# Performance work log

Hardware: AMD Instinct MI355X
Metric: run time of the kernel (lower is better)

The kernel has to match this reference:

```python
import jax, jax.numpy as jnp
import numpy as np

N = 50000      # nodes
E = 800000     # edges
D = 128        # input_dim
H = 128        # hidden_dim
C = 10         # num_classes
G = 1024       # graphs in batch
EPS = 1e-5     # BatchNorm eps


def setup_inputs() -> dict:
    key = jax.random.key(0)
    ks = jax.random.split(key, 16)
    p = lambda k, shape: (jax.random.normal(k, shape, dtype=jnp.float32) * 0.05)
    inp = {
        "x": jax.random.normal(ks[0], (N, D), dtype=jnp.float32),
        "edge_index": jax.random.randint(ks[1], (2, E), 0, N, dtype=jnp.int64),
        "batch": jnp.sort(jax.random.randint(ks[2], (N,), 0, G, dtype=jnp.int64)),
        # GraphConv l: out = x @ w_root + segment_sum(x[src])[dst] @ w_rel + b (PyG GraphConv, aggr='add')
        "w_root1": p(ks[3], (D, H)), "w_rel1": p(ks[4], (D, H)), "b1": p(ks[5], (H,)),
        "w_root2": p(ks[6], (H, H)), "w_rel2": p(ks[7], (H, H)), "b2": p(ks[8], (H,)),
        "w_root3": p(ks[9], (H, H)), "w_rel3": p(ks[10], (H, H)), "b3": p(ks[11], (H,)),
        "g1": jnp.ones((H,), jnp.float32), "be1": jnp.zeros((H,), jnp.float32),
        "g2": jnp.ones((H,), jnp.float32), "be2": jnp.zeros((H,), jnp.float32),
        "g3": jnp.ones((H,), jnp.float32), "be3": jnp.zeros((H,), jnp.float32),
        "w_cls": p(ks[12], (H, C)), "b_cls": p(ks[13], (C,)),
    }
    return inp


def _graph_conv(x, src, dst, w_root, w_rel, b):
    # PyG GraphConv: lin_root(x) + lin_rel(sum_{j in N(i)} x_j) + bias
    agg = jax.ops.segment_sum(x[src], dst, num_segments=N)
    return x @ w_root + agg @ w_rel + b


def _batch_norm(x, gamma, beta):
    mean = jnp.mean(x, axis=0)
    var = jnp.var(x, axis=0)
    return (x - mean) * jax.lax.rsqrt(var + EPS) * gamma + beta


def reference(x, edge_index, batch,
              w_root1, w_rel1, b1, w_root2, w_rel2, b2, w_root3, w_rel3, b3,
              g1, be1, g2, be2, g3, be3, w_cls, b_cls):
    src, dst = edge_index[0], edge_index[1]
    h = jax.nn.relu(_batch_norm(_graph_conv(x, src, dst, w_root1, w_rel1, b1), g1, be1))
    h = jax.nn.relu(_batch_norm(_graph_conv(h, src, dst, w_root2, w_rel2, b2), g2, be2))
    h = _batch_norm(_graph_conv(h, src, dst, w_root3, w_rel3, b3), g3, be3)
    # global_mean_pool over graph ids
    sums = jax.ops.segment_sum(h, batch, num_segments=G)
    counts = jax.ops.segment_sum(jnp.ones((N,), h.dtype), batch, num_segments=G)
    pooled = sums / jnp.maximum(counts, 1.0)[:, None]
    # dropout is identity in eval mode
    return pooled @ w_cls + b_cls
```

## Files before the change

### kernel.cpp

```cpp
#include <hip/hip_runtime.h>


constexpr int   NN   = 50000;
constexpr int   NE   = 800000;
constexpr int   DH   = 128;
constexpr int   NC   = 10;
constexpr int   NG   = 1024;
constexpr float EPSV = 1e-5f;
constexpr int   NB   = (NN + 255) / 256;
constexpr int   NBUK = (NN + 255) / 256;
constexpr int   BCAP = 5120;
constexpr int   EPB  = 8192;
constexpr int   CSB  = (NE + EPB - 1) / EPB;
constexpr int   NSLOT= 32;

typedef __attribute__((ext_vector_type(8))) short bf16x8;
typedef __attribute__((ext_vector_type(4))) float f32x4;

__device__ __forceinline__ float bflo(unsigned u) { return __uint_as_float(u << 16); }
__device__ __forceinline__ float bfhi(unsigned u) { return __uint_as_float(u & 0xffff0000u); }
__device__ __forceinline__ unsigned short f2bf(float f) {
    unsigned u = __float_as_uint(f);
    return (unsigned short)((u + 0x7fffu + ((u >> 16) & 1u)) >> 16);
}
__device__ __forceinline__ unsigned pk2(float a, float b) {
    return (unsigned)f2bf(a) | ((unsigned)f2bf(b) << 16);
}

__global__ __launch_bounds__(256) void coarse_scatter_kernel(
    const int* __restrict__ src, const int* __restrict__ dst,
    int* __restrict__ bukCnt, int2* __restrict__ pairs)
{
    __shared__ int cnt[NBUK], base[NBUK], cur[NBUK];
    const int tid = threadIdx.x;
    const int e0 = blockIdx.x * EPB;
    const int n  = min(EPB, NE - e0);

    for (int b = tid; b < NBUK; b += 256) cnt[b] = 0;
    __syncthreads();
    for (int i = tid; i < n; i += 256)
        atomicAdd(&cnt[dst[e0 + i] >> 8], 1);
    __syncthreads();
    for (int b = tid; b < NBUK; b += 256) {
        base[b] = (cnt[b] > 0) ? atomicAdd(&bukCnt[b], cnt[b]) : 0;
        cur[b] = 0;
    }
    __syncthreads();
    for (int i = tid; i < n; i += 256) {
        int d = dst[e0 + i], s = src[e0 + i];
        int b = d >> 8;
        int r = atomicAdd(&cur[b], 1);
        int p = base[b] + r;
        if (p >= BCAP) p = BCAP - 1;
        pairs[(size_t)b * BCAP + p] = make_int2(s, d);
    }
}

__global__ __launch_bounds__(256) void deg_from_pairs_kernel(
    const int2* __restrict__ pairs, const int* __restrict__ bukCnt,
    int* __restrict__ deg)
{
    __shared__ int cnt[256];
    const int b = blockIdx.x;
    const int tid = threadIdx.x;
    cnt[tid] = 0;
    __syncthreads();
    const int n = min(bukCnt[b], BCAP);
    const int2* p = pairs + (size_t)b * BCAP;
    for (int i = tid; i < n; i += 256)
        atomicAdd(&cnt[p[i].y & 255], 1);
    __syncthreads();
    int node = b * 256 + tid;
    if (node < NN) deg[node] = cnt[tid];
}

__global__ __launch_bounds__(256) void fine_scatter_kernel(
    const int2* __restrict__ pairs, const int* __restrict__ bukCnt,
    int* __restrict__ cursor, int* __restrict__ csr_src)
{
    const int b = blockIdx.x;
    const int tid = threadIdx.x;
    const int n = min(bukCnt[b], BCAP);
    const int2* p = pairs + (size_t)b * BCAP;
    for (int i = tid; i < n; i += 256) {
        int2 e = p[i];
        int pos = atomicAdd(&cursor[e.y], 1);
        csr_src[pos] = e.x;
    }
}

__global__ __launch_bounds__(256) void psum_kernel(
    const int* __restrict__ deg, int* __restrict__ bsum)
{
    int t = threadIdx.x;
    int i = blockIdx.x * 256 + t;
    int d = (i < NN) ? deg[i] : 0;
#pragma unroll
    for (int off = 32; off > 0; off >>= 1) d += __shfl_down(d, off, 64);
    __shared__ int w4[4];
    if ((t & 63) == 0) w4[t >> 6] = d;
    __syncthreads();
    if (t == 0) bsum[blockIdx.x] = w4[0] + w4[1] + w4[2] + w4[3];
}

__global__ __launch_bounds__(256) void scan_bsums_kernel(
    const int* __restrict__ bsum, int* __restrict__ bbase)
{
    __shared__ int tmp[256];
    int t = threadIdx.x;
    int v = (t < NB) ? bsum[t] : 0;
    tmp[t] = v;
    __syncthreads();
    for (int off = 1; off < 256; off <<= 1) {
        int u = (t >= off) ? tmp[t - off] : 0;
        __syncthreads();
        tmp[t] += u;
        __syncthreads();
    }
    if (t < NB) bbase[t] = tmp[t] - v;
}

__global__ __launch_bounds__(256) void offsets_kernel(
    const int* __restrict__ deg, const int* __restrict__ bbase,
    int* __restrict__ offsets, int* __restrict__ cursor)
{
    __shared__ int tmp[256];
    int t = threadIdx.x;
    int i = blockIdx.x * 256 + t;
    int d = (i < NN) ? deg[i] : 0;
    tmp[t] = d;
    __syncthreads();
    for (int off = 1; off < 256; off <<= 1) {
        int u = (t >= off) ? tmp[t - off] : 0;
        __syncthreads();
        tmp[t] += u;
        __syncthreads();
    }
    int incl = tmp[t];
    int base = bbase[blockIdx.x];
    if (i < NN) {
        int o = base + incl - d;
        offsets[i] = o;
        cursor[i]  = o;
        if (i == NN - 1) offsets[NN] = base + incl;
    }
}

__global__ __launch_bounds__(256) void convert_x_kernel(
    const float* __restrict__ x, unsigned short* __restrict__ xb)
{
    int i = blockIdx.x * 256 + threadIdx.x;
    if (i >= NN * DH / 8) return;
    const float4* p = reinterpret_cast<const float4*>(x + (size_t)i * 8);
    float4 v0 = p[0], v1 = p[1];
    uint4 o;
    o.x = pk2(v0.x, v0.y); o.y = pk2(v0.z, v0.w);
    o.z = pk2(v1.x, v1.y); o.w = pk2(v1.z, v1.w);
    *reinterpret_cast<uint4*>(xb + (size_t)i * 8) = o;
}

__global__ __launch_bounds__(256) void transpose_w_kernel(
    const float* __restrict__ w0, const float* __restrict__ w1,
    const float* __restrict__ w2, const float* __restrict__ w3,
    const float* __restrict__ w4, const float* __restrict__ w5,
    unsigned short* __restrict__ t0, unsigned short* __restrict__ t1,
    unsigned short* __restrict__ t2, unsigned short* __restrict__ t3,
    unsigned short* __restrict__ t4, unsigned short* __restrict__ t5)
{
    const float* srcs[6] = {w0, w1, w2, w3, w4, w5};
    unsigned short* dsts[6] = {t0, t1, t2, t3, t4, t5};
    int m = blockIdx.x >> 4;
    int sub = blockIdx.x & 15;
    const float* s = srcs[m];
    unsigned short* d = dsts[m];
    for (int it = 0; it < 4; ++it) {
        int i = sub * 1024 + it * 256 + threadIdx.x;
        int c = i & 127, k = i >> 7;
        d[c * 128 + k] = f2bf(s[k * 128 + c]);
    }
}

template <bool TRANSFORM>
__global__ __launch_bounds__(256) void aggregate_kernel(
    const unsigned short* __restrict__ xb, const int* __restrict__ offsets,
    const int* __restrict__ csr_src, const float* __restrict__ sc,
    const float* __restrict__ sh, unsigned short* __restrict__ aggb)
{
    int tid = blockIdx.x * 256 + threadIdx.x;
    int node = tid >> 4;
    if (node >= NN) return;
    int c8 = (tid & 15) * 8;

    float scv[8], shv[8];
    if (TRANSFORM) {
        float4 a = *reinterpret_cast<const float4*>(sc + c8);
        float4 b = *reinterpret_cast<const float4*>(sc + c8 + 4);
        scv[0]=a.x; scv[1]=a.y; scv[2]=a.z; scv[3]=a.w;
        scv[4]=b.x; scv[5]=b.y; scv[6]=b.z; scv[7]=b.w;
        float4 c = *reinterpret_cast<const float4*>(sh + c8);
        float4 d = *reinterpret_cast<const float4*>(sh + c8 + 4);
        shv[0]=c.x; shv[1]=c.y; shv[2]=c.z; shv[3]=c.w;
        shv[4]=d.x; shv[5]=d.y; shv[6]=d.z; shv[7]=d.w;
    }

    float acc[8] = {0.f,0.f,0.f,0.f,0.f,0.f,0.f,0.f};
    auto addv = [&](uint4 v) {
        float f[8] = {bflo(v.x), bfhi(v.x), bflo(v.y), bfhi(v.y),
                      bflo(v.z), bfhi(v.z), bflo(v.w), bfhi(v.w)};
#pragma unroll
        for (int j = 0; j < 8; ++j) {
            float t = TRANSFORM ? fmaxf(fmaf(f[j], scv[j], shv[j]), 0.f) : f[j];
            acc[j] += t;
        }
    };

    int beg = offsets[node], end = offsets[node + 1];
    int e = beg;
    for (; e + 3 < end; e += 4) {
        int s0 = csr_src[e],     s1 = csr_src[e + 1];
        int s2 = csr_src[e + 2], s3 = csr_src[e + 3];
        uint4 v0 = *reinterpret_cast<const uint4*>(xb + (size_t)s0 * DH + c8);
        uint4 v1 = *reinterpret_cast<const uint4*>(xb + (size_t)s1 * DH + c8);
        uint4 v2 = *reinterpret_cast<const uint4*>(xb + (size_t)s2 * DH + c8);
        uint4 v3 = *reinterpret_cast<const uint4*>(xb + (size_t)s3 * DH + c8);
        addv(v0); addv(v1); addv(v2); addv(v3);
    }
    for (; e < end; ++e)
        addv(*reinterpret_cast<const uint4*>(xb + (size_t)csr_src[e] * DH + c8));

    uint4 o;
    o.x = pk2(acc[0], acc[1]); o.y = pk2(acc[2], acc[3]);
    o.z = pk2(acc[4], acc[5]); o.w = pk2(acc[6], acc[7]);
    *reinterpret_cast<uint4*>(aggb + (size_t)node * DH + c8) = o;
}

template <bool TRANSFORM>
__global__ __launch_bounds__(256, 4) void gemm_mfma_kernel(
    const unsigned short* __restrict__ Xb, const unsigned short* __restrict__ Ab,
    const unsigned short* __restrict__ Wrt, const unsigned short* __restrict__ Wlt,
    const float* __restrict__ bias, const float* __restrict__ scIn,
    const float* __restrict__ shIn, unsigned short* __restrict__ OUTb,
    float* __restrict__ stats)
{
    __shared__ unsigned short sW[128][136];
    __shared__ float sScale[DH], sShift[DH];

    const int tid  = threadIdx.x;
    const int lane = tid & 63;
    const int wave = tid >> 6;
    const int row0 = blockIdx.x * 64;
    const int wrow = wave * 16;
    const int l15  = lane & 15;
    const int lk   = (lane >> 4) * 8;

    if (TRANSFORM && tid < DH) {
        sScale[tid] = scIn[tid];
        sShift[tid] = shIn[tid];
    }
#pragma unroll
    for (int i = 0; i < 8; ++i) {
        int f = i * 256 + tid;
        int c = f >> 4;
        int ks = (f & 15) * 8;
        *reinterpret_cast<uint4*>(&sW[c][ks]) =
            *reinterpret_cast<const uint4*>(Wrt + c * 128 + ks);
    }

    f32x4 acc[8];
#pragma unroll
    for (int nt = 0; nt < 8; ++nt) acc[nt] = (f32x4){0.f, 0.f, 0.f, 0.f};

    const int arow = row0 + wrow + l15;
    const bool valid = arow < NN;
    const unsigned short* xptr = Xb + (size_t)arow * DH + lk;
    const unsigned short* aptr = Ab + (size_t)arow * DH + lk;

    uint4 pre[4];
#pragma unroll
    for (int t = 0; t < 4; ++t)
        pre[t] = valid ? *reinterpret_cast<const uint4*>(xptr + t * 32)
                       : make_uint4(0u, 0u, 0u, 0u);

    __syncthreads();

#pragma unroll
    for (int t = 0; t < 4; ++t) {
        uint4 v = pre[t];
        if (TRANSFORM) {
            int cb = t * 32 + lk;
            float f[8] = {bflo(v.x), bfhi(v.x), bflo(v.y), bfhi(v.y),
                          bflo(v.z), bfhi(v.z), bflo(v.w), bfhi(v.w)};
#pragma unroll
            for (int j = 0; j < 8; ++j)
                f[j] = fmaxf(fmaf(f[j], sScale[cb + j], sShift[cb + j]), 0.f);
            v.x = pk2(f[0], f[1]); v.y = pk2(f[2], f[3]);
            v.z = pk2(f[4], f[5]); v.w = pk2(f[6], f[7]);
        }
        bf16x8 a = *reinterpret_cast<bf16x8*>(&v);
        const int kb = t * 32;
#pragma unroll
        for (int nt = 0; nt < 8; ++nt) {
            bf16x8 b = *reinterpret_cast<const bf16x8*>(&sW[nt * 16 + l15][kb + lk]);
            acc[nt] = __builtin_amdgcn_mfma_f32_16x16x32_bf16(a, b, acc[nt], 0, 0, 0);
        }
    }

#pragma unroll
    for (int t = 0; t < 4; ++t)
        pre[t] = valid ? *reinterpret_cast<const uint4*>(aptr + t * 32)
                       : make_uint4(0u, 0u, 0u, 0u);

    __syncthreads();
#pragma unroll
    for (int i = 0; i < 8; ++i) {
        int f = i * 256 + tid;
        int c = f >> 4;
        int ks = (f & 15) * 8;
        *reinterpret_cast<uint4*>(&sW[c][ks]) =
            *reinterpret_cast<const uint4*>(Wlt + c * 128 + ks);
    }
    __syncthreads();

#pragma unroll
    for (int t = 0; t < 4; ++t) {
        uint4 v = pre[t];
        bf16x8 a = *reinterpret_cast<bf16x8*>(&v);
        const int kb = t * 32;
#pragma unroll
        for (int nt = 0; nt < 8; ++nt) {
            bf16x8 b = *reinterpret_cast<const bf16x8*>(&sW[nt * 16 + l15][kb + lk]);
            acc[nt] = __builtin_amdgcn_mfma_f32_16x16x32_bf16(a, b, acc[nt], 0, 0, 0);
        }
    }

    float s_[8] = {0,0,0,0,0,0,0,0}, q_[8] = {0,0,0,0,0,0,0,0};
#pragma unroll
    for (int nt = 0; nt < 8; ++nt) {
        float bvn = bias[nt * 16 + l15];
#pragma unroll
        for (int r = 0; r < 4; ++r) {
            int orow = row0 + wrow + ((lane >> 4) << 2) + r;
            float o = acc[nt][r] + bvn;
            if (orow < NN) {
                OUTb[(size_t)orow * DH + nt * 16 + l15] = f2bf(o);
                s_[nt] += o;
                q_[nt] += o * o;
            }
        }
    }
#pragma unroll
    for (int nt = 0; nt < 8; ++nt) {
        s_[nt] += __shfl_xor(s_[nt], 16, 64);
        s_[nt] += __shfl_xor(s_[nt], 32, 64);
        q_[nt] += __shfl_xor(q_[nt], 16, 64);
        q_[nt] += __shfl_xor(q_[nt], 32, 64);
    }
    __syncthreads();
    float* ldsS = reinterpret_cast<float*>(&sW[0][0]);
    float* ldsQ = ldsS + 512;
    if (lane < 16) {
#pragma unroll
        for (int nt = 0; nt < 8; ++nt) {
            ldsS[wave * DH + nt * 16 + l15] = s_[nt];
            ldsQ[wave * DH + nt * 16 + l15] = q_[nt];
        }
    }
    __syncthreads();
    if (tid < DH) {
        float s = ldsS[tid] + ldsS[DH + tid] + ldsS[2 * DH + tid] + ldsS[3 * DH + tid];
        float q = ldsQ[tid] + ldsQ[DH + tid] + ldsQ[2 * DH + tid] + ldsQ[3 * DH + tid];
        float* slot = stats + (size_t)(blockIdx.x & (NSLOT - 1)) * 256;
        atomicAdd(&slot[tid], s);
        atomicAdd(&slot[128 + tid], q);
    }
}

__global__ __launch_bounds__(128) void finalize_kernel(
    const float* __restrict__ stats, const float* __restrict__ gamma,
    const float* __restrict__ beta, float* __restrict__ sc,
    float* __restrict__ sh)
{
    int j = threadIdx.x;
    float s = 0.f, q = 0.f;
#pragma unroll 8
    for (int sl = 0; sl < NSLOT; ++sl) {
        s += stats[sl * 256 + j];
        q += stats[sl * 256 + 128 + j];
    }
    float mean = s * (1.f / NN);
    float var  = q * (1.f / NN) - mean * mean;
    float sf = rsqrtf(var + EPSV) * gamma[j];
    sc[j] = sf;
    sh[j] = beta[j] - mean * sf;
}

__global__ __launch_bounds__(256) void ghist_kernel(
    const int* __restrict__ batch, int* __restrict__ gdeg)
{
    int n = blockIdx.x * 256 + threadIdx.x;
    if (n < NN) atomicAdd(&gdeg[batch[n]], 1);
}

__global__ __launch_bounds__(1024) void gscan_kernel(
    const int* __restrict__ gdeg, int* __restrict__ goff)
{
    __shared__ int part[1024];
    int t = threadIdx.x;
    part[t] = gdeg[t];
    __syncthreads();
    for (int off = 1; off < 1024; off <<= 1) {
        int v = (t >= off) ? part[t - off] : 0;
        __syncthreads();
        part[t] += v;
        __syncthreads();
    }
    goff[t + 1] = part[t];
    if (t == 0) goff[0] = 0;
}

__global__ __launch_bounds__(128) void pool_classify_kernel(
    const unsigned short* __restrict__ Hb, const int* __restrict__ goff,
    const float* __restrict__ sc, const float* __restrict__ sh,
    const float* __restrict__ wcls, const float* __restrict__ bcls,
    float* __restrict__ out)
{
    __shared__ float pl[DH];
    int g = blockIdx.x;
    int j = threadIdx.x;
    int beg = goff[g], end = goff[g + 1];
    float s = 0.f;
    for (int n = beg; n < end; ++n)
        s += bflo((unsigned)Hb[(size_t)n * DH + j]);
    float cnt = (float)(end - beg);
    pl[j] = (s * sc[j] + cnt * sh[j]) / fmaxf(cnt, 1.f);
    __syncthreads();
    if (j < NC) {
        float v = bcls[j];
#pragma unroll 16
        for (int k = 0; k < DH; ++k) v += pl[k] * wcls[k * NC + j];
        out[(size_t)g * NC + j] = v;
    }
}

extern "C" void kernel_launch(void* const* d_in, const int* in_sizes, int n_in,
                              void* d_out, int out_size, void* d_ws, size_t ws_size,
                              hipStream_t stream)
{
    const float* x    = (const float*)d_in[0];
    const int*   ei   = (const int*)d_in[1];
    const int*   batch= (const int*)d_in[2];
    const float* wr1  = (const float*)d_in[3];
    const float* wl1  = (const float*)d_in[4];
    const float* b1   = (const float*)d_in[5];
    const float* wr2  = (const float*)d_in[6];
    const float* wl2  = (const float*)d_in[7];
    const float* b2   = (const float*)d_in[8];
    const float* wr3  = (const float*)d_in[9];
    const float* wl3  = (const float*)d_in[10];
    const float* b3   = (const float*)d_in[11];
    const float* g1   = (const float*)d_in[12];
    const float* be1  = (const float*)d_in[13];
    const float* g2   = (const float*)d_in[14];
    const float* be2  = (const float*)d_in[15];
    const float* g3   = (const float*)d_in[16];
    const float* be3  = (const float*)d_in[17];
    const float* wcls = (const float*)d_in[18];
    const float* bcls = (const float*)d_in[19];
    float* out = (float*)d_out;

    const int* srcp = ei;
    const int* dstp = ei + NE;

    char* ws = (char*)d_ws;
    const size_t featB16 = (size_t)NN * DH * sizeof(unsigned short);
    size_t off = 0;
    auto alloc = [&](size_t bytes) {
        void* p = ws + off;
        off += (bytes + 255) & ~(size_t)255;
        return p;
    };
    unsigned short* xb    = (unsigned short*)alloc(featB16);
    unsigned short* aggb  = (unsigned short*)alloc(featB16);
    unsigned short* hAb   = (unsigned short*)alloc(featB16);
    unsigned short* hBb   = (unsigned short*)alloc(featB16);
    unsigned short* wrt1  = (unsigned short*)alloc(DH * DH * 2);
    unsigned short* wlt1  = (unsigned short*)alloc(DH * DH * 2);
    unsigned short* wrt2  = (unsigned short*)alloc(DH * DH * 2);
    unsigned short* wlt2  = (unsigned short*)alloc(DH * DH * 2);
    unsigned short* wrt3  = (unsigned short*)alloc(DH * DH * 2);
    unsigned short* wlt3  = (unsigned short*)alloc(DH * DH * 2);
    float* statsAll = (float*)alloc(3 * NSLOT * 256 * sizeof(float));
    float* stats1 = statsAll;
    float* stats2 = statsAll + NSLOT * 256;
    float* stats3 = statsAll + 2 * NSLOT * 256;
    int*   deg     = (int*)alloc(NN * sizeof(int));
    int*   offsets = (int*)alloc((NN + 1) * sizeof(int));
    int*   cursor  = (int*)alloc(NN * sizeof(int));
    int*   csr_src = (int*)alloc(NE * sizeof(int));
    int2*  pairs   = (int2*)alloc((size_t)NBUK * BCAP * sizeof(int2));
    int*   bukCnt  = (int*)alloc(NBUK * sizeof(int));
    int*   gdeg    = (int*)alloc(NG * sizeof(int));
    int*   goff    = (int*)alloc((NG + 1) * sizeof(int));
    int*   bsum    = (int*)alloc(NB * sizeof(int));
    int*   bbase   = (int*)alloc(NB * sizeof(int));
    float* sc1 = (float*)alloc(DH * 4); float* sh1 = (float*)alloc(DH * 4);
    float* sc2 = (float*)alloc(DH * 4); float* sh2 = (float*)alloc(DH * 4);
    float* sc3 = (float*)alloc(DH * 4); float* sh3 = (float*)alloc(DH * 4);

    const int nodeBlocks = (NN + 255) / 256;
    const int aggBlocks  = (NN * 16 + 255) / 256;
    const int gemmBlocks = (NN + 63) / 64;
    const int cvtBlocks  = (NN * DH / 8 + 255) / 256;

    hipMemsetAsync(statsAll, 0, 3 * NSLOT * 256 * sizeof(float), stream);

    hipMemsetAsync(bukCnt, 0, NBUK * sizeof(int), stream);
    coarse_scatter_kernel<<<CSB, 256, 0, stream>>>(srcp, dstp, bukCnt, pairs);
    deg_from_pairs_kernel<<<NBUK, 256, 0, stream>>>(pairs, bukCnt, deg);
    psum_kernel<<<NB, 256, 0, stream>>>(deg, bsum);
    scan_bsums_kernel<<<1, 256, 0, stream>>>(bsum, bbase);
    offsets_kernel<<<NB, 256, 0, stream>>>(deg, bbase, offsets, cursor);
    fine_scatter_kernel<<<NBUK, 256, 0, stream>>>(pairs, bukCnt, cursor, csr_src);

    hipMemsetAsync(gdeg, 0, NG * sizeof(int), stream);
    ghist_kernel<<<nodeBlocks, 256, 0, stream>>>(batch, gdeg);
    gscan_kernel<<<1, 1024, 0, stream>>>(gdeg, goff);

    convert_x_kernel<<<cvtBlocks, 256, 0, stream>>>(x, xb);
    transpose_w_kernel<<<96, 256, 0, stream>>>(wr1, wl1, wr2, wl2, wr3, wl3,
                                               wrt1, wlt1, wrt2, wlt2, wrt3, wlt3);

    aggregate_kernel<false><<<aggBlocks, 256, 0, stream>>>(xb, offsets, csr_src, nullptr, nullptr, aggb);
    gemm_mfma_kernel<false><<<gemmBlocks, 256, 0, stream>>>(xb, aggb, wrt1, wlt1, b1, nullptr, nullptr, hAb, stats1);
    finalize_kernel<<<1, 128, 0, stream>>>(stats1, g1, be1, sc1, sh1);

    aggregate_kernel<true><<<aggBlocks, 256, 0, stream>>>(hAb, offsets, csr_src, sc1, sh1, aggb);
    gemm_mfma_kernel<true><<<gemmBlocks, 256, 0, stream>>>(hAb, aggb, wrt2, wlt2, b2, sc1, sh1, hBb, stats2);
    finalize_kernel<<<1, 128, 0, stream>>>(stats2, g2, be2, sc2, sh2);

    aggregate_kernel<true><<<aggBlocks, 256, 0, stream>>>(hBb, offsets, csr_src, sc2, sh2, aggb);
    gemm_mfma_kernel<true><<<gemmBlocks, 256, 0, stream>>>(hBb, aggb, wrt3, wlt3, b3, sc2, sh2, hAb, stats3);
    finalize_kernel<<<1, 128, 0, stream>>>(stats3, g3, be3, sc3, sh3);

    pool_classify_kernel<<<NG, 128, 0, stream>>>(hAb, goff, sc3, sh3, wcls, bcls, out);
}
```

Baseline: 259.9 us.

## Slice aggregation by feature quarters and compute graph offsets by binary search

The aggregate kernel now gives each block 64 nodes and one 32-column quarter of the features, with 4 threads per node instead of 16 threads covering all 128 columns. This narrows each gather row to 64 bytes and should improve cache locality per slice, at the cost of reading the CSR indices four times. Graph offsets are now found by a binary search over the sorted batch array, which replaces the histogram, memset and scan kernels with a single small launch. That search depends on batch being sorted, as the reference input is.

```diff
diff --git a/kernel.cpp b/kernel.cpp
--- a/kernel.cpp
+++ b/kernel.cpp
@@ -146,6 +146,19 @@
     }
 }
 
+__global__ __launch_bounds__(256) void goff_kernel(
+    const int* __restrict__ batch, int* __restrict__ goff)
+{
+    int g = blockIdx.x * 256 + threadIdx.x;
+    if (g > NG) return;
+    int lo = 0, hi = NN;
+    while (lo < hi) {
+        int mid = (lo + hi) >> 1;
+        if (batch[mid] < g) lo = mid + 1; else hi = mid;
+    }
+    goff[g] = lo;
+}
+
 __global__ __launch_bounds__(256) void convert_x_kernel(
     const float* __restrict__ x, unsigned short* __restrict__ xb)
 {
@@ -186,10 +199,10 @@
     const int* __restrict__ csr_src, const float* __restrict__ sc,
     const float* __restrict__ sh, unsigned short* __restrict__ aggb)
 {
-    int tid = blockIdx.x * 256 + threadIdx.x;
-    int node = tid >> 4;
+    const int slice = blockIdx.x & 3;
+    const int node  = (blockIdx.x >> 2) * 64 + (threadIdx.x >> 2);
     if (node >= NN) return;
-    int c8 = (tid & 15) * 8;
+    const int c8 = slice * 32 + (threadIdx.x & 3) * 8;
 
     float scv[8], shv[8];
     if (TRANSFORM) {
@@ -392,30 +405,6 @@
     float sf = rsqrtf(var + EPSV) * gamma[j];
     sc[j] = sf;
     sh[j] = beta[j] - mean * sf;
-}
-
-__global__ __launch_bounds__(256) void ghist_kernel(
-    const int* __restrict__ batch, int* __restrict__ gdeg)
-{
-    int n = blockIdx.x * 256 + threadIdx.x;
-    if (n < NN) atomicAdd(&gdeg[batch[n]], 1);
-}
-
-__global__ __launch_bounds__(1024) void gscan_kernel(
-    const int* __restrict__ gdeg, int* __restrict__ goff)
-{
-    __shared__ int part[1024];
-    int t = threadIdx.x;
-    part[t] = gdeg[t];
-    __syncthreads();
-    for (int off = 1; off < 1024; off <<= 1) {
-        int v = (t >= off) ? part[t - off] : 0;
-        __syncthreads();
-        part[t] += v;
-        __syncthreads();
-    }
-    goff[t + 1] = part[t];
-    if (t == 0) goff[0] = 0;
 }
 
 __global__ __launch_bounds__(128) void pool_classify_kernel(
@@ -499,7 +488,6 @@
     int*   csr_src = (int*)alloc(NE * sizeof(int));
     int2*  pairs   = (int2*)alloc((size_t)NBUK * BCAP * sizeof(int2));
     int*   bukCnt  = (int*)alloc(NBUK * sizeof(int));
-    int*   gdeg    = (int*)alloc(NG * sizeof(int));
     int*   goff    = (int*)alloc((NG + 1) * sizeof(int));
     int*   bsum    = (int*)alloc(NB * sizeof(int));
     int*   bbase   = (int*)alloc(NB * sizeof(int));
@@ -507,8 +495,7 @@
     float* sc2 = (float*)alloc(DH * 4); float* sh2 = (float*)alloc(DH * 4);
     float* sc3 = (float*)alloc(DH * 4); float* sh3 = (float*)alloc(DH * 4);
 
-    const int nodeBlocks = (NN + 255) / 256;
-    const int aggBlocks  = (NN * 16 + 255) / 256;
+    const int aggBlocks  = ((NN + 63) / 64) * 4;
     const int gemmBlocks = (NN + 63) / 64;
     const int cvtBlocks  = (NN * DH / 8 + 255) / 256;
 
@@ -522,9 +509,7 @@
     offsets_kernel<<<NB, 256, 0, stream>>>(deg, bbase, offsets, cursor);
     fine_scatter_kernel<<<NBUK, 256, 0, stream>>>(pairs, bukCnt, cursor, csr_src);
 
-    hipMemsetAsync(gdeg, 0, NG * sizeof(int), stream);
-    ghist_kernel<<<nodeBlocks, 256, 0, stream>>>(batch, gdeg);
-    gscan_kernel<<<1, 1024, 0, stream>>>(gdeg, goff);
+    goff_kernel<<<(NG + 256) / 256, 256, 0, stream>>>(batch, goff);
 
     convert_x_kernel<<<cvtBlocks, 256, 0, stream>>>(x, xb);
     transpose_w_kernel<<<96, 256, 0, stream>>>(wr1, wl1, wr2, wl2, wr3, wl3,
```

After: 283.5 us. 1.09x slower.
